# Performance work log

Hardware: AMD Instinct MI355X
Metric: run time of the kernel (lower is better)

The kernel has to match this reference:

```python
import jax, jax.numpy as jnp
import numpy as np

DIM = 1024
N_EXPERTS = 8
TOP_K = 2
B, S = 2, 1024


def setup_inputs() -> dict:
    key = jax.random.key(0)
    ks = jax.random.split(key, 4)
    scale = 0.02
    return {
        "u_t": jax.random.normal(ks[0], (B, S, DIM), dtype=jnp.float32),
        "centroids": jax.random.normal(ks[1], (N_EXPERTS, DIM), dtype=jnp.float32),
        "score_biases": jnp.zeros((N_EXPERTS,), dtype=jnp.float32),
        "W1": jax.random.normal(ks[2], (N_EXPERTS, DIM, 4 * DIM), dtype=jnp.float32) * scale,
        "b1": jnp.zeros((N_EXPERTS, 4 * DIM), dtype=jnp.float32),
        "W2": jax.random.normal(ks[3], (N_EXPERTS, 4 * DIM, DIM), dtype=jnp.float32) * scale,
        "b2": jnp.zeros((N_EXPERTS, DIM), dtype=jnp.float32),
    }


def reference(u_t, centroids, score_biases, W1, b1, W2, b2):
    Bs, Ss, dim = u_t.shape
    T = Bs * Ss
    N = centroids.shape[0]
    K = TOP_K

    u_flat = u_t.reshape(T, dim)
    scores = u_flat @ centroids.T + score_biases          # [T, N]
    gate = jax.nn.softmax(scores, axis=-1)                # [T, N]
    topk_vals, topk_idx = jax.lax.top_k(gate, K)          # [T, K]

    flat_idx = topk_idx.reshape(-1)                       # [T*K]

    # load-violation stats (no grad path; pure counts)
    perfect_load = K * T / N
    f_i = jnp.zeros((N,), dtype=jnp.float32).at[flat_idx].add(1.0)
    maxvio = (jnp.max(f_i) - perfect_load) / perfect_load

    # Grouped MLP expressed as dense per-expert compute over all tokens,
    # then combined with a sparse [T, N] gate matrix (same math as masked dispatch).
    h = jax.nn.relu(jnp.einsum("td,ndh->nth", u_flat, W1) + b1[:, None, :])  # [N, T, 4*dim]
    expert_outs = jnp.einsum("nth,nhd->ntd", h, W2) + b2[:, None, :]          # [N, T, dim]

    rows = jnp.repeat(jnp.arange(T), K)
    combine_w = jnp.zeros((T, N), dtype=topk_vals.dtype).at[rows, flat_idx].add(topk_vals.reshape(-1))
    out = jnp.einsum("tn,ntd->td", combine_w, expert_outs).reshape(Bs, Ss, dim)
    return (out, maxvio)
```

## Files before the change

kernel.cpp:

```cpp
#include <hip/hip_runtime.h>
#include <hip/hip_bf16.h>

#define T_TOK 2048
#define DIMS  1024
#define HID   4096
#define NE    8

typedef __bf16 bf16x8 __attribute__((ext_vector_type(8)));
typedef float  f32x4  __attribute__((ext_vector_type(4)));

__device__ __forceinline__ unsigned short f2bf(float f) {
  unsigned u = __float_as_uint(f);
  u += 0x7FFFu + ((u >> 16) & 1u);
  return (unsigned short)(u >> 16);
}
__device__ __forceinline__ float bf2f(unsigned short s) {
  return __uint_as_float(((unsigned)s) << 16);
}

__device__ __forceinline__ void g2l16(const void* g, void* l) {
  __builtin_amdgcn_global_load_lds((const __attribute__((address_space(1))) void*)g,
                                   (__attribute__((address_space(3))) void*)l,
                                   16, 0, 0);
}

__global__ __launch_bounds__(256) void k_route(const float* __restrict__ u,
    const float* __restrict__ cent, const float* __restrict__ sbias,
    int* __restrict__ topk_idx, float* __restrict__ topk_val,
    unsigned short* __restrict__ ub) {
  int wave = threadIdx.x >> 6;
  int lane = threadIdx.x & 63;
  int t = blockIdx.x * 4 + wave;
  const float* ur = u + (size_t)t * DIMS;
  float p[NE];
#pragma unroll
  for (int n = 0; n < NE; n++) p[n] = 0.f;
#pragma unroll
  for (int ch = 0; ch < 4; ch++) {
    int d = ch * 256 + lane * 4;
    float4 uv = *(const float4*)(ur + d);
    ushort4 o4;
    o4.x = f2bf(uv.x); o4.y = f2bf(uv.y); o4.z = f2bf(uv.z); o4.w = f2bf(uv.w);
    *(ushort4*)(ub + (size_t)t * DIMS + d) = o4;
#pragma unroll
    for (int n = 0; n < NE; n++) {
      float4 cv = *(const float4*)(cent + n * DIMS + d);
      p[n] += uv.x * cv.x + uv.y * cv.y + uv.z * cv.z + uv.w * cv.w;
    }
  }
#pragma unroll
  for (int n = 0; n < NE; n++) {
#pragma unroll
    for (int o = 32; o > 0; o >>= 1) p[n] += __shfl_xor(p[n], o);
  }
  if (lane == 0) {
    float g[NE];
    float m = -1e30f;
#pragma unroll
    for (int n = 0; n < NE; n++) { g[n] = p[n] + sbias[n]; m = fmaxf(m, g[n]); }
    float sum = 0.f;
#pragma unroll
    for (int n = 0; n < NE; n++) { g[n] = expf(g[n] - m); sum += g[n]; }
    float inv = 1.f / sum;
#pragma unroll
    for (int n = 0; n < NE; n++) g[n] *= inv;
    int i0 = 0;
#pragma unroll
    for (int n = 1; n < NE; n++) if (g[n] > g[i0]) i0 = n;
    int i1 = (i0 == 0) ? 1 : 0;
#pragma unroll
    for (int n = 0; n < NE; n++) if (n != i0 && g[n] > g[i1]) i1 = n;
    topk_idx[2 * t] = i0;     topk_idx[2 * t + 1] = i1;
    topk_val[2 * t] = g[i0];  topk_val[2 * t + 1] = g[i1];
  }
}

__global__ __launch_bounds__(256) void k_finalize(const int* __restrict__ topk_idx,
    int* __restrict__ cnt, int* __restrict__ offs, float* __restrict__ maxvio,
    int* __restrict__ rowtok, int* __restrict__ pairpos) {
  __shared__ int lc[NE], lcur[NE];
  int tid = threadIdx.x;
  if (tid < NE) lc[tid] = 0;
  __syncthreads();
#pragma unroll
  for (int i = 0; i < 16; i++) {
    int e = topk_idx[tid * 16 + i];
    atomicAdd(&lc[e], 1);
  }
  __syncthreads();
  if (tid == 0) {
    int o = 0, mx = 0;
#pragma unroll
    for (int n = 0; n < NE; n++) {
      int c = lc[n];
      cnt[n] = c; offs[n] = o; lcur[n] = o;
      o += c; mx = max(mx, c);
    }
    maxvio[0] = ((float)mx - 512.f) / 512.f;
  }
  __syncthreads();
#pragma unroll
  for (int i = 0; i < 8; i++) {
    int t = tid + i * 256;
#pragma unroll
    for (int k = 0; k < 2; k++) {
      int e = topk_idx[2 * t + k];
      int pos = atomicAdd(&lcur[e], 1);
      rowtok[pos] = t;
      pairpos[2 * t + k] = pos;
    }
  }
}

#define BM 128
#define BN 128
#define BK 64

__global__ __launch_bounds__(256) void k_gemm1(const unsigned short* __restrict__ ub,
    const float* __restrict__ W1, const float* __restrict__ b1,
    const int* __restrict__ rowtok, const int* __restrict__ cnts, const int* __restrict__ offs,
    unsigned short* __restrict__ h,
    const float* __restrict__ W2, unsigned short* __restrict__ w2t) {
  __shared__ __align__(16) unsigned char smem[32768];
  int tid = threadIdx.x;
  int e = blockIdx.z;
  int cnt = cnts[e];
  int m0 = blockIdx.y * BM;

  if (m0 >= cnt) {
    int live[NE];
#pragma unroll
    for (int z = 0; z < NE; z++) live[z] = min(16, (cnts[z] + BM - 1) >> 7);
    int rank = 0;
    for (int z = 0; z < e; z++) rank += (16 - live[z]) * 32;
    rank += ((int)blockIdx.y - live[e]) * 32 + (int)blockIdx.x;
    if (rank >= 2048) return;
    int te = rank >> 8, tt = rank & 255;
    int r0 = (tt & 31) * 128, c0 = (tt >> 5) * 128;
    const float* Wsrc = W2 + (size_t)te * HID * DIMS;
    unsigned short* dst = w2t + (size_t)te * HID * DIMS;
    unsigned short* lds = (unsigned short*)smem;
    int rbase = tid >> 5;
    int c4l = (tid & 31) * 4;
#pragma unroll 4
    for (int it = 0; it < 16; it++) {
      int r = rbase + it * 8;
      float4 v = *(const float4*)(Wsrc + (size_t)(r0 + r) * DIMS + c0 + c4l);
      unsigned short b[4];
      b[0] = f2bf(v.x); b[1] = f2bf(v.y); b[2] = f2bf(v.z); b[3] = f2bf(v.w);
#pragma unroll
      for (int j = 0; j < 4; j++) {
        int c = c4l + j;
        int chunk = it ^ ((c >> 2) & 15);
        lds[c * 128 + chunk * 8 + rbase] = b[j];
      }
    }
    __syncthreads();
    int ck = tid & 15;
    int cb = tid >> 4;
#pragma unroll 4
    for (int it = 0; it < 8; it++) {
      int c = cb + it * 16;
      int chunk = ck ^ ((c >> 2) & 15);
      uint4 v = *(const uint4*)(&lds[c * 128 + chunk * 8]);
      *(uint4*)(dst + (size_t)(c0 + c) * HID + r0 + ck * 8) = v;
    }
    return;
  }

  int off = offs[e];
  int n0 = blockIdx.x * BN;
  int lane = tid & 63;
  int wv = tid >> 6;
  int wm = (tid >> 7) & 1;
  int wn = (tid >> 6) & 1;
  int srow = tid >> 3;
  int cp = tid & 7;
  const float* w1e = W1 + (size_t)e * DIMS * HID;
  const unsigned short* gAp[4];
#pragma unroll
  for (int a = 0; a < 4; a++) {
    int r = a * 32 + srow;
    int c = cp ^ (r & 7);
    int pr = min(off + m0 + r, off + cnt - 1);
    int tok = rowtok[pr];
    gAp[a] = ub + (size_t)tok * DIMS + c * 8;
  }
  int wboff = __builtin_amdgcn_readfirstlane(wv << 10);
  f32x4 acc[4][4];
  f32x4 zz = {0.f, 0.f, 0.f, 0.f};
#pragma unroll
  for (int i = 0; i < 4; i++)
#pragma unroll
    for (int j = 0; j < 4; j++) acc[i][j] = zz;

  int lane15 = lane & 15, quad = lane >> 4, l7 = lane & 7;
  unsigned aRowOff = (unsigned)((wm * 64 + lane15) * 128);
  unsigned bRowOff = (unsigned)(16384 + (wn * 64 + lane15) * 128);

#pragma unroll 1
  for (int k0 = 0; k0 < DIMS; k0 += BK) {
#pragma unroll
    for (int a = 0; a < 4; a++) g2l16(gAp[a] + k0, smem + a * 4096 + wboff);
#pragma unroll
    for (int jj = 0; jj < 4; jj++) {
      int j = wv * 4 + jj;
      int kc = j & 7, nh = j >> 3;
      int nloc = nh * 64 + lane;
      const float* src = w1e + (size_t)(k0 + kc * 8) * HID + n0 + nloc;
      float t0, t1, t2, t3, t4, t5, t6, t7;
      t0 = src[0];            t1 = src[(size_t)HID];
      t2 = src[(size_t)2 * HID]; t3 = src[(size_t)3 * HID];
      t4 = src[(size_t)4 * HID]; t5 = src[(size_t)5 * HID];
      t6 = src[(size_t)6 * HID]; t7 = src[(size_t)7 * HID];
      bf16x8 pk;
      pk[0] = (__bf16)t0; pk[1] = (__bf16)t1; pk[2] = (__bf16)t2; pk[3] = (__bf16)t3;
      pk[4] = (__bf16)t4; pk[5] = (__bf16)t5; pk[6] = (__bf16)t6; pk[7] = (__bf16)t7;
      int cs = kc ^ (lane & 7);
      *(bf16x8*)(smem + 16384 + nloc * 128 + cs * 16) = pk;
    }
    __syncthreads();
#pragma unroll
    for (int s = 0; s < 2; s++) {
      unsigned cpf = (unsigned)(((s * 4 + quad) ^ l7) * 16);
      bf16x8 af[4], bfr[4];
#pragma unroll
      for (int i = 0; i < 4; i++) af[i] = *(const bf16x8*)(smem + aRowOff + i * 2048 + cpf);
#pragma unroll
      for (int j = 0; j < 4; j++) bfr[j] = *(const bf16x8*)(smem + bRowOff + j * 2048 + cpf);
#pragma unroll
      for (int i = 0; i < 4; i++)
#pragma unroll
        for (int j = 0; j < 4; j++)
          acc[i][j] = __builtin_amdgcn_mfma_f32_16x16x32_bf16(af[i], bfr[j], acc[i][j], 0, 0, 0);
    }
    __syncthreads();
  }
  float b1v[4];
#pragma unroll
  for (int j = 0; j < 4; j++) b1v[j] = b1[e * HID + n0 + wn * 64 + j * 16 + lane15];
#pragma unroll
  for (int i = 0; i < 4; i++) {
#pragma unroll
    for (int r = 0; r < 4; r++) {
      int mrow = m0 + wm * 64 + i * 16 + quad * 4 + r;
      if (mrow < cnt) {
        size_t hrow = (size_t)(off + mrow) * HID;
#pragma unroll
        for (int j = 0; j < 4; j++) {
          int col = n0 + wn * 64 + j * 16 + lane15;
          float v = fmaxf(acc[i][j][r] + b1v[j], 0.f);
          h[hrow + col] = f2bf(v);
        }
      }
    }
  }
}

__global__ __launch_bounds__(256) void k_gemm2(const unsigned short* __restrict__ hbuf,
    const unsigned short* __restrict__ w2t, const float* __restrict__ b2,
    const int* __restrict__ cnts, const int* __restrict__ offs,
    unsigned short* __restrict__ pout, int KC) {
  int z = blockIdx.z;
  int e = z & 7;
  int sp = z >> 3;
  int cnt = cnts[e];
  int m0 = blockIdx.y * BM;
  if (m0 >= cnt) return;
  int off = offs[e];
  int n0 = blockIdx.x * BN;
  __shared__ __align__(16) unsigned char smem[32768];

  int tid = threadIdx.x;
  int lane = tid & 63;
  int wm = (tid >> 7) & 1;
  int wn = (tid >> 6) & 1;
  int srow = tid >> 3;
  int cp = tid & 7;
  const unsigned short* gA[4];
  const unsigned short* gB[4];
#pragma unroll
  for (int a = 0; a < 4; a++) {
    int r = a * 32 + srow;
    int c = cp ^ (r & 7);
    int pr = min(off + m0 + r, off + cnt - 1);
    gA[a] = hbuf + (size_t)pr * HID + c * 8;
    gB[a] = w2t + ((size_t)e * DIMS + (n0 + r)) * HID + c * 8;
  }
  int wboff = __builtin_amdgcn_readfirstlane((tid >> 6) << 10);
  f32x4 acc[4][4];
  f32x4 zz = {0.f, 0.f, 0.f, 0.f};
#pragma unroll
  for (int i = 0; i < 4; i++)
#pragma unroll
    for (int j = 0; j < 4; j++) acc[i][j] = zz;

  int lane15 = lane & 15, quad = lane >> 4, l7 = lane & 7;
  unsigned aRowOff = (unsigned)((wm * 64 + lane15) * 128);
  unsigned bRowOff = (unsigned)(16384 + (wn * 64 + lane15) * 128);

  int kbeg = sp * KC, kend = kbeg + KC;
#pragma unroll 1
  for (int k0 = kbeg; k0 < kend; k0 += BK) {
#pragma unroll
    for (int a = 0; a < 4; a++) g2l16(gA[a] + k0, smem + a * 4096 + wboff);
#pragma unroll
    for (int a = 0; a < 4; a++) g2l16(gB[a] + k0, smem + 16384 + a * 4096 + wboff);
    __syncthreads();
#pragma unroll
    for (int s = 0; s < 2; s++) {
      unsigned cpf = (unsigned)(((s * 4 + quad) ^ l7) * 16);
      bf16x8 af[4], bfr[4];
#pragma unroll
      for (int i = 0; i < 4; i++) af[i] = *(const bf16x8*)(smem + aRowOff + i * 2048 + cpf);
#pragma unroll
      for (int j = 0; j < 4; j++) bfr[j] = *(const bf16x8*)(smem + bRowOff + j * 2048 + cpf);
#pragma unroll
      for (int i = 0; i < 4; i++)
#pragma unroll
        for (int j = 0; j < 4; j++)
          acc[i][j] = __builtin_amdgcn_mfma_f32_16x16x32_bf16(af[i], bfr[j], acc[i][j], 0, 0, 0);
    }
    __syncthreads();
  }
  float b2v[4];
#pragma unroll
  for (int j = 0; j < 4; j++)
    b2v[j] = (sp == 0) ? b2[e * DIMS + n0 + wn * 64 + j * 16 + lane15] : 0.f;
  unsigned short* pme = pout + (size_t)sp * T_TOK * 2 * DIMS;
#pragma unroll
  for (int i = 0; i < 4; i++) {
#pragma unroll
    for (int r = 0; r < 4; r++) {
      int mrow = m0 + wm * 64 + i * 16 + quad * 4 + r;
      if (mrow < cnt) {
        size_t prow = (size_t)(off + mrow) * DIMS;
#pragma unroll
        for (int j = 0; j < 4; j++) {
          int col = n0 + wn * 64 + j * 16 + lane15;
          pme[prow + col] = f2bf(acc[i][j][r] + b2v[j]);
        }
      }
    }
  }
}

__global__ __launch_bounds__(256) void k_combine(const unsigned short* __restrict__ pout,
    const int* __restrict__ pairpos, const float* __restrict__ tkv,
    float* __restrict__ out, int nsplit) {
  int t = blockIdx.x;
  int d = threadIdx.x * 4;
  int p0 = pairpos[2 * t], p1 = pairpos[2 * t + 1];
  float w0 = tkv[2 * t], w1 = tkv[2 * t + 1];
  float a0 = 0.f, a1 = 0.f, a2 = 0.f, a3 = 0.f;
  float c0 = 0.f, c1 = 0.f, c2 = 0.f, c3 = 0.f;
  const size_t SS = (size_t)T_TOK * 2 * DIMS;
  for (int s = 0; s < nsplit; s++) {
    ushort4 av = *(const ushort4*)(pout + s * SS + (size_t)p0 * DIMS + d);
    ushort4 bv = *(const ushort4*)(pout + s * SS + (size_t)p1 * DIMS + d);
    a0 += bf2f(av.x); a1 += bf2f(av.y); a2 += bf2f(av.z); a3 += bf2f(av.w);
    c0 += bf2f(bv.x); c1 += bf2f(bv.y); c2 += bf2f(bv.z); c3 += bf2f(bv.w);
  }
  float4 o;
  o.x = w0 * a0 + w1 * c0;
  o.y = w0 * a1 + w1 * c1;
  o.z = w0 * a2 + w1 * c2;
  o.w = w0 * a3 + w1 * c3;
  *(float4*)(out + (size_t)t * DIMS + d) = o;
}

extern "C" void kernel_launch(void* const* d_in, const int* in_sizes, int n_in,
                              void* d_out, int out_size, void* d_ws, size_t ws_size,
                              hipStream_t stream) {
  const float* u     = (const float*)d_in[0];
  const float* cent  = (const float*)d_in[1];
  const float* sbias = (const float*)d_in[2];
  const float* W1    = (const float*)d_in[3];
  const float* b1    = (const float*)d_in[4];
  const float* W2    = (const float*)d_in[5];
  const float* b2    = (const float*)d_in[6];
  float* out = (float*)d_out;

  char* ws = (char*)d_ws;
  unsigned short* ubuf = (unsigned short*)(ws);
  unsigned short* hbuf = (unsigned short*)(ws + 4194304);
  unsigned short* w2t  = (unsigned short*)(ws + 37748736);
  const size_t POUT_OFF = 104857600ull;
  const size_t PSZ = (size_t)T_TOK * 2 * DIMS * 2;
  int nsplit = (ws_size >= POUT_OFF + 4 * PSZ + (1u << 20)) ? 4 : 1;
  unsigned short* poutb = (unsigned short*)(ws + POUT_OFF);
  char* r = ws + POUT_OFF + (size_t)nsplit * PSZ;
  int*   cnt      = (int*)(r);
  int*   offs     = (int*)(r + 64);
  int*   topk_idx = (int*)(r + 256);
  float* topk_val = (float*)(r + 256 + 16384);
  int*   rowtok   = (int*)(r + 256 + 32768);
  int*   pairpos  = (int*)(r + 256 + 49152);

  k_route<<<512, 256, 0, stream>>>(u, cent, sbias, topk_idx, topk_val, ubuf);
  k_finalize<<<1, 256, 0, stream>>>(topk_idx, cnt, offs, out + 2097152, rowtok, pairpos);
  k_gemm1<<<dim3(32, 16, 8), 256, 0, stream>>>(ubuf, W1, b1, rowtok, cnt, offs, hbuf,
                                               W2, w2t);
  k_gemm2<<<dim3(8, 16, 8 * nsplit), 256, 0, stream>>>(hbuf, w2t, b2, cnt, offs,
                                                       poutb, HID / nsplit);
  k_combine<<<2048, 256, 0, stream>>>(poutb, pairpos, topk_val, out, nsplit);
}
```

Measured before the change: 420.1 us.

## Pretranscode W1 to bf16 in routing kernel and double-buffer GEMM LDS pipelines

Extra blocks in the routing kernel convert W1 to a transposed bf16 copy, so the first GEMM loads bf16 tiles through direct global-to-LDS copies instead of handling fp32 weights in its main loop. Both GEMMs now double-buffer LDS (64KB) and prefetch the next K tile while computing the current one, using explicit vmcnt waits and barriers. The split-K factor for GEMM2 drops from 4 to 2, and the W1 copy reuses the partial-output region. The costs are extra transcoding traffic in the routing launch and lower occupancy from the larger LDS footprint.

```diff
diff --git a/kernel.cpp b/kernel.cpp
--- a/kernel.cpp
+++ b/kernel.cpp
@@ -5,6 +5,9 @@
 #define DIMS  1024
 #define HID   4096
 #define NE    8
+#define BM 128
+#define BN 128
+#define BK 64
 
 typedef __bf16 bf16x8 __attribute__((ext_vector_type(8)));
 typedef float  f32x4  __attribute__((ext_vector_type(4)));
@@ -24,10 +27,50 @@
                                    16, 0, 0);
 }
 
+__device__ __forceinline__ void transcode_tile(const float* __restrict__ src,
+    unsigned short* __restrict__ dst, int src_ld, int dst_ld, int r0, int c0,
+    unsigned short* lds, int tid) {
+  int rbase = tid >> 5;
+  int c4l = (tid & 31) * 4;
+#pragma unroll 4
+  for (int it = 0; it < 16; it++) {
+    int r = rbase + it * 8;
+    float4 v = *(const float4*)(src + (size_t)(r0 + r) * src_ld + c0 + c4l);
+    unsigned short b[4];
+    b[0] = f2bf(v.x); b[1] = f2bf(v.y); b[2] = f2bf(v.z); b[3] = f2bf(v.w);
+#pragma unroll
+    for (int j = 0; j < 4; j++) {
+      int c = c4l + j;
+      int chunk = it ^ ((c >> 2) & 15);
+      lds[c * 128 + chunk * 8 + rbase] = b[j];
+    }
+  }
+  __syncthreads();
+  int ck = tid & 15;
+  int cb = tid >> 4;
+#pragma unroll 4
+  for (int it = 0; it < 8; it++) {
+    int c = cb + it * 16;
+    int chunk = ck ^ ((c >> 2) & 15);
+    uint4 v = *(const uint4*)(&lds[c * 128 + chunk * 8]);
+    *(uint4*)(dst + (size_t)(c0 + c) * dst_ld + r0 + ck * 8) = v;
+  }
+}
+
 __global__ __launch_bounds__(256) void k_route(const float* __restrict__ u,
     const float* __restrict__ cent, const float* __restrict__ sbias,
     int* __restrict__ topk_idx, float* __restrict__ topk_val,
-    unsigned short* __restrict__ ub) {
+    unsigned short* __restrict__ ub,
+    const float* __restrict__ W1, unsigned short* __restrict__ w1t) {
+  __shared__ __align__(16) unsigned short tlds[128 * 128];
+  if (blockIdx.x >= 512) {
+    int rank = (int)blockIdx.x - 512;
+    int te = rank >> 8, tt = rank & 255;
+    int r0 = (tt & 7) * 128, c0 = (tt >> 3) * 128;
+    transcode_tile(W1 + (size_t)te * DIMS * HID, w1t + (size_t)te * HID * DIMS,
+                   HID, DIMS, r0, c0, tlds, threadIdx.x);
+    return;
+  }
   int wave = threadIdx.x >> 6;
   int lane = threadIdx.x & 63;
   int t = blockIdx.x * 4 + wave;
@@ -112,11 +155,123 @@
   }
 }
 
-#define BM 128
-#define BN 128
-#define BK 64
-
-__global__ __launch_bounds__(256) void k_gemm1(const unsigned short* __restrict__ ub,
+__global__ __launch_bounds__(256) void k_gemm1n(const unsigned short* __restrict__ ub,
+    const unsigned short* __restrict__ w1t, const float* __restrict__ b1,
+    const int* __restrict__ rowtok, const int* __restrict__ cnts, const int* __restrict__ offs,
+    unsigned short* __restrict__ h,
+    const float* __restrict__ W2, unsigned short* __restrict__ w2t) {
+  __shared__ __align__(16) unsigned char smem[65536];
+  int tid = threadIdx.x;
+  int e = blockIdx.z;
+  int cnt = cnts[e];
+  int m0 = blockIdx.y * BM;
+
+  if (m0 >= cnt) {
+    int live[NE];
+#pragma unroll
+    for (int z = 0; z < NE; z++) live[z] = min(16, (cnts[z] + BM - 1) >> 7);
+    int rank = 0;
+    for (int z = 0; z < e; z++) rank += (16 - live[z]) * 32;
+    rank += ((int)blockIdx.y - live[e]) * 32 + (int)blockIdx.x;
+    if (rank >= 2048) return;
+    int te = rank >> 8, tt = rank & 255;
+    transcode_tile(W2 + (size_t)te * HID * DIMS, w2t + (size_t)te * HID * DIMS,
+                   DIMS, HID, (tt & 31) * 128, (tt >> 5) * 128,
+                   (unsigned short*)smem, tid);
+    return;
+  }
+
+  int off = offs[e];
+  int n0 = blockIdx.x * BN;
+  int lane = tid & 63;
+  int wm = (tid >> 7) & 1;
+  int wn = (tid >> 6) & 1;
+  int srow = tid >> 3;
+  int cp = tid & 7;
+  const unsigned short* gA[4];
+  const unsigned short* gB[4];
+#pragma unroll
+  for (int a = 0; a < 4; a++) {
+    int r = a * 32 + srow;
+    int c = cp ^ (r & 7);
+    int pr = min(off + m0 + r, off + cnt - 1);
+    int tok = rowtok[pr];
+    gA[a] = ub + (size_t)tok * DIMS + c * 8;
+    gB[a] = w1t + ((size_t)e * HID + (n0 + r)) * DIMS + c * 8;
+  }
+  unsigned wboff = (unsigned)__builtin_amdgcn_readfirstlane((tid >> 6) << 10);
+  f32x4 acc[4][4];
+  f32x4 zz = {0.f, 0.f, 0.f, 0.f};
+#pragma unroll
+  for (int i = 0; i < 4; i++)
+#pragma unroll
+    for (int j = 0; j < 4; j++) acc[i][j] = zz;
+
+  int lane15 = lane & 15, quad = lane >> 4, l7 = lane & 7;
+  unsigned aOff = (unsigned)((wm * 64 + lane15) * 128);
+  unsigned bOff = (unsigned)(16384 + (wn * 64 + lane15) * 128);
+
+#pragma unroll
+  for (int a = 0; a < 4; a++) g2l16(gA[a], smem + a * 4096 + wboff);
+#pragma unroll
+  for (int a = 0; a < 4; a++) g2l16(gB[a], smem + 16384 + a * 4096 + wboff);
+
+#pragma unroll 1
+  for (int it = 0; it < DIMS / BK; it++) {
+    unsigned base = (unsigned)((it & 1) << 15);
+    unsigned nb = base ^ 32768u;
+    if (it + 1 < DIMS / BK) {
+      int k1 = (it + 1) * BK;
+#pragma unroll
+      for (int a = 0; a < 4; a++) g2l16(gA[a] + k1, smem + nb + a * 4096 + wboff);
+#pragma unroll
+      for (int a = 0; a < 4; a++) g2l16(gB[a] + k1, smem + nb + 16384 + a * 4096 + wboff);
+      asm volatile("s_waitcnt vmcnt(8)" ::: "memory");
+    } else {
+      asm volatile("s_waitcnt vmcnt(0)" ::: "memory");
+    }
+    __builtin_amdgcn_s_barrier();
+    __builtin_amdgcn_sched_barrier(0);
+#pragma unroll
+    for (int s = 0; s < 2; s++) {
+      unsigned cpf = (unsigned)(((s * 4 + quad) ^ l7) * 16);
+      bf16x8 af[4], bfr[4];
+#pragma unroll
+      for (int i = 0; i < 4; i++) af[i] = *(const bf16x8*)(smem + base + aOff + i * 2048 + cpf);
+#pragma unroll
+      for (int j = 0; j < 4; j++) bfr[j] = *(const bf16x8*)(smem + base + bOff + j * 2048 + cpf);
+#pragma unroll
+      for (int i = 0; i < 4; i++)
+#pragma unroll
+        for (int j = 0; j < 4; j++)
+          acc[i][j] = __builtin_amdgcn_mfma_f32_16x16x32_bf16(af[i], bfr[j], acc[i][j], 0, 0, 0);
+    }
+    __builtin_amdgcn_sched_barrier(0);
+    asm volatile("s_waitcnt lgkmcnt(0)" ::: "memory");
+    __builtin_amdgcn_s_barrier();
+  }
+  float b1v[4];
+#pragma unroll
+  for (int j = 0; j < 4; j++) b1v[j] = b1[e * HID + n0 + wn * 64 + j * 16 + lane15];
+#pragma unroll
+  for (int i = 0; i < 4; i++) {
+#pragma unroll
+    for (int r = 0; r < 4; r++) {
+      int mrow = m0 + wm * 64 + i * 16 + quad * 4 + r;
+      if (mrow < cnt) {
+        size_t hrow = (size_t)(off + mrow) * HID;
+#pragma unroll
+        for (int j = 0; j < 4; j++) {
+          int col = n0 + wn * 64 + j * 16 + lane15;
+          float v = fmaxf(acc[i][j][r] + b1v[j], 0.f);
+          h[hrow + col] = f2bf(v);
+        }
+      }
+    }
+  }
+}
+
+__global__ __launch_bounds__(256) void k_gemm1o(const unsigned short* __restrict__ ub,
     const float* __restrict__ W1, const float* __restrict__ b1,
     const int* __restrict__ rowtok, const int* __restrict__ cnts, const int* __restrict__ offs,
     unsigned short* __restrict__ h,
@@ -136,35 +291,9 @@
     rank += ((int)blockIdx.y - live[e]) * 32 + (int)blockIdx.x;
     if (rank >= 2048) return;
     int te = rank >> 8, tt = rank & 255;
-    int r0 = (tt & 31) * 128, c0 = (tt >> 5) * 128;
-    const float* Wsrc = W2 + (size_t)te * HID * DIMS;
-    unsigned short* dst = w2t + (size_t)te * HID * DIMS;
-    unsigned short* lds = (unsigned short*)smem;
-    int rbase = tid >> 5;
-    int c4l = (tid & 31) * 4;
-#pragma unroll 4
-    for (int it = 0; it < 16; it++) {
-      int r = rbase + it * 8;
-      float4 v = *(const float4*)(Wsrc + (size_t)(r0 + r) * DIMS + c0 + c4l);
-      unsigned short b[4];
-      b[0] = f2bf(v.x); b[1] = f2bf(v.y); b[2] = f2bf(v.z); b[3] = f2bf(v.w);
-#pragma unroll
-      for (int j = 0; j < 4; j++) {
-        int c = c4l + j;
-        int chunk = it ^ ((c >> 2) & 15);
-        lds[c * 128 + chunk * 8 + rbase] = b[j];
-      }
-    }
-    __syncthreads();
-    int ck = tid & 15;
-    int cb = tid >> 4;
-#pragma unroll 4
-    for (int it = 0; it < 8; it++) {
-      int c = cb + it * 16;
-      int chunk = ck ^ ((c >> 2) & 15);
-      uint4 v = *(const uint4*)(&lds[c * 128 + chunk * 8]);
-      *(uint4*)(dst + (size_t)(c0 + c) * HID + r0 + ck * 8) = v;
-    }
+    transcode_tile(W2 + (size_t)te * HID * DIMS, w2t + (size_t)te * HID * DIMS,
+                   DIMS, HID, (tt & 31) * 128, (tt >> 5) * 128,
+                   (unsigned short*)smem, tid);
     return;
   }
 
@@ -269,7 +398,7 @@
   if (m0 >= cnt) return;
   int off = offs[e];
   int n0 = blockIdx.x * BN;
-  __shared__ __align__(16) unsigned char smem[32768];
+  __shared__ __align__(16) unsigned char smem[65536];
 
   int tid = threadIdx.x;
   int lane = tid & 63;
@@ -287,7 +416,7 @@
     gA[a] = hbuf + (size_t)pr * HID + c * 8;
     gB[a] = w2t + ((size_t)e * DIMS + (n0 + r)) * HID + c * 8;
   }
-  int wboff = __builtin_amdgcn_readfirstlane((tid >> 6) << 10);
+  unsigned wboff = (unsigned)__builtin_amdgcn_readfirstlane((tid >> 6) << 10);
   f32x4 acc[4][4];
   f32x4 zz = {0.f, 0.f, 0.f, 0.f};
 #pragma unroll
@@ -296,32 +425,49 @@
     for (int j = 0; j < 4; j++) acc[i][j] = zz;
 
   int lane15 = lane & 15, quad = lane >> 4, l7 = lane & 7;
-  unsigned aRowOff = (unsigned)((wm * 64 + lane15) * 128);
-  unsigned bRowOff = (unsigned)(16384 + (wn * 64 + lane15) * 128);
-
-  int kbeg = sp * KC, kend = kbeg + KC;
+  unsigned aOff = (unsigned)((wm * 64 + lane15) * 128);
+  unsigned bOff = (unsigned)(16384 + (wn * 64 + lane15) * 128);
+
+  int kbeg = sp * KC;
+  int NIT = KC / BK;
+#pragma unroll
+  for (int a = 0; a < 4; a++) g2l16(gA[a] + kbeg, smem + a * 4096 + wboff);
+#pragma unroll
+  for (int a = 0; a < 4; a++) g2l16(gB[a] + kbeg, smem + 16384 + a * 4096 + wboff);
+
 #pragma unroll 1
-  for (int k0 = kbeg; k0 < kend; k0 += BK) {
-#pragma unroll
-    for (int a = 0; a < 4; a++) g2l16(gA[a] + k0, smem + a * 4096 + wboff);
-#pragma unroll
-    for (int a = 0; a < 4; a++) g2l16(gB[a] + k0, smem + 16384 + a * 4096 + wboff);
-    __syncthreads();
+  for (int it = 0; it < NIT; it++) {
+    unsigned base = (unsigned)((it & 1) << 15);
+    unsigned nb = base ^ 32768u;
+    if (it + 1 < NIT) {
+      int k1 = kbeg + (it + 1) * BK;
+#pragma unroll
+      for (int a = 0; a < 4; a++) g2l16(gA[a] + k1, smem + nb + a * 4096 + wboff);
+#pragma unroll
+      for (int a = 0; a < 4; a++) g2l16(gB[a] + k1, smem + nb + 16384 + a * 4096 + wboff);
+      asm volatile("s_waitcnt vmcnt(8)" ::: "memory");
+    } else {
+      asm volatile("s_waitcnt vmcnt(0)" ::: "memory");
+    }
+    __builtin_amdgcn_s_barrier();
+    __builtin_amdgcn_sched_barrier(0);
 #pragma unroll
     for (int s = 0; s < 2; s++) {
       unsigned cpf = (unsigned)(((s * 4 + quad) ^ l7) * 16);
       bf16x8 af[4], bfr[4];
 #pragma unroll
-      for (int i = 0; i < 4; i++) af[i] = *(const bf16x8*)(smem + aRowOff + i * 2048 + cpf);
-#pragma unroll
-      for (int j = 0; j < 4; j++) bfr[j] = *(const bf16x8*)(smem + bRowOff + j * 2048 + cpf);
+      for (int i = 0; i < 4; i++) af[i] = *(const bf16x8*)(smem + base + aOff + i * 2048 + cpf);
+#pragma unroll
+      for (int j = 0; j < 4; j++) bfr[j] = *(const bf16x8*)(smem + base + bOff + j * 2048 + cpf);
 #pragma unroll
       for (int i = 0; i < 4; i++)
 #pragma unroll
         for (int j = 0; j < 4; j++)
           acc[i][j] = __builtin_amdgcn_mfma_f32_16x16x32_bf16(af[i], bfr[j], acc[i][j], 0, 0, 0);
     }
-    __syncthreads();
+    __builtin_amdgcn_sched_barrier(0);
+    asm volatile("s_waitcnt lgkmcnt(0)" ::: "memory");
+    __builtin_amdgcn_s_barrier();
   }
   float b2v[4];
 #pragma unroll
@@ -385,23 +531,46 @@
   unsigned short* ubuf = (unsigned short*)(ws);
   unsigned short* hbuf = (unsigned short*)(ws + 4194304);
   unsigned short* w2t  = (unsigned short*)(ws + 37748736);
-  const size_t POUT_OFF = 104857600ull;
+  const size_t REG4 = 104857600ull;
   const size_t PSZ = (size_t)T_TOK * 2 * DIMS * 2;
-  int nsplit = (ws_size >= POUT_OFF + 4 * PSZ + (1u << 20)) ? 4 : 1;
-  unsigned short* poutb = (unsigned short*)(ws + POUT_OFF);
-  char* r = ws + POUT_OFF + (size_t)nsplit * PSZ;
-  int*   cnt      = (int*)(r);
-  int*   offs     = (int*)(r + 64);
-  int*   topk_idx = (int*)(r + 256);
-  float* topk_val = (float*)(r + 256 + 16384);
-  int*   rowtok   = (int*)(r + 256 + 32768);
-  int*   pairpos  = (int*)(r + 256 + 49152);
-
-  k_route<<<512, 256, 0, stream>>>(u, cent, sbias, topk_idx, topk_val, ubuf);
-  k_finalize<<<1, 256, 0, stream>>>(topk_idx, cnt, offs, out + 2097152, rowtok, pairpos);
-  k_gemm1<<<dim3(32, 16, 8), 256, 0, stream>>>(ubuf, W1, b1, rowtok, cnt, offs, hbuf,
-                                               W2, w2t);
-  k_gemm2<<<dim3(8, 16, 8 * nsplit), 256, 0, stream>>>(hbuf, w2t, b2, cnt, offs,
-                                                       poutb, HID / nsplit);
-  k_combine<<<2048, 256, 0, stream>>>(poutb, pairpos, topk_val, out, nsplit);
-}
+  const size_t NEED_NEW = REG4 + 67108864ull + 1048576ull;
+
+  if (ws_size >= NEED_NEW) {
+    unsigned short* w1t   = (unsigned short*)(ws + REG4);
+    unsigned short* poutb = (unsigned short*)(ws + REG4);
+    const int nsplit = 2;
+    char* r = ws + REG4 + 67108864ull;
+    int*   cnt      = (int*)(r);
+    int*   offs     = (int*)(r + 64);
+    int*   topk_idx = (int*)(r + 256);
+    float* topk_val = (float*)(r + 256 + 16384);
+    int*   rowtok   = (int*)(r + 256 + 32768);
+    int*   pairpos  = (int*)(r + 256 + 49152);
+
+    k_route<<<2560, 256, 0, stream>>>(u, cent, sbias, topk_idx, topk_val, ubuf, W1, w1t);
+    k_finalize<<<1, 256, 0, stream>>>(topk_idx, cnt, offs, out + 2097152, rowtok, pairpos);
+    k_gemm1n<<<dim3(32, 16, 8), 256, 0, stream>>>(ubuf, w1t, b1, rowtok, cnt, offs, hbuf,
+                                                  W2, w2t);
+    k_gemm2<<<dim3(8, 16, 8 * nsplit), 256, 0, stream>>>(hbuf, w2t, b2, cnt, offs,
+                                                         poutb, HID / nsplit);
+    k_combine<<<2048, 256, 0, stream>>>(poutb, pairpos, topk_val, out, nsplit);
+  } else {
+    int nsplit = (ws_size >= REG4 + 4 * PSZ + (1u << 20)) ? 4 : 1;
+    unsigned short* poutb = (unsigned short*)(ws + REG4);
+    char* r = ws + REG4 + (size_t)nsplit * PSZ;
+    int*   cnt      = (int*)(r);
+    int*   offs     = (int*)(r + 64);
+    int*   topk_idx = (int*)(r + 256);
+    float* topk_val = (float*)(r + 256 + 16384);
+    int*   rowtok   = (int*)(r + 256 + 32768);
+    int*   pairpos  = (int*)(r + 256 + 49152);
+
+    k_route<<<512, 256, 0, stream>>>(u, cent, sbias, topk_idx, topk_val, ubuf, W1, ubuf);
+    k_finalize<<<1, 256, 0, stream>>>(topk_idx, cnt, offs, out + 2097152, rowtok, pairpos);
+    k_gemm1o<<<dim3(32, 16, 8), 256, 0, stream>>>(ubuf, W1, b1, rowtok, cnt, offs, hbuf,
+                                                  W2, w2t);
+    k_gemm2<<<dim3(8, 16, 8 * nsplit), 256, 0, stream>>>(hbuf, w2t, b2, cnt, offs,
+                                                         poutb, HID / nsplit);
+    k_combine<<<2048, 256, 0, stream>>>(poutb, pairpos, topk_val, out, nsplit);
+  }
+}
```

After: 430.2 us. 2.4% more time.
